# Optimization experiments

Hardware: AMD Instinct MI355X
Metric: run time of the kernel (lower is better)

Reference implementation:

```python
import jax, jax.numpy as jnp
import numpy as np

B, N = 32, 1024
NUM = B * N
DIMS = [(1, 128, 8), (128, 128, 8), (128, 64, 16), (64, 64, 16), (64, 32, 1)]  # (cin, cout, heads)

def _edges():
    # bidirectional chain per batch element, offset by N per graph (as in torch forward)
    a = np.arange(N - 1)
    offs = (np.arange(B) * N)[:, None]
    src = np.concatenate([(a[None] + offs).ravel(), (a[None] + 1 + offs).ravel()])
    dst = np.concatenate([(a[None] + 1 + offs).ravel(), (a[None] + offs).ravel()])
    return jnp.asarray(src, jnp.int32), jnp.asarray(dst, jnp.int32)

def _conv(x, src, dst, Wm, bm, Ws, bs, att):
    # PyG GeneralConv: directed msg, additive attention, aggr='add', head-mean, + lin_self
    h, cout = att.shape
    m = (x @ Wm + bm)[src].reshape(-1, h, cout)          # [E, H, C] edge messages
    m = jnp.where(m > 0, m, 0.01 * m)                    # F.leaky_relu default slope 0.01
    alpha = jnp.einsum('ehc,hc->eh', m, att)             # [E, H] attention logits
    amax = jax.ops.segment_max(alpha, dst, num_segments=NUM)
    ex = jnp.exp(alpha - amax[dst])
    den = jax.ops.segment_sum(ex, dst, num_segments=NUM)
    w = ex / (den[dst] + 1e-16)                          # segment softmax over incoming edges
    agg = jax.ops.segment_sum(m * w[:, :, None], dst, num_segments=NUM)  # [NUM, H, C]
    return agg.mean(axis=1) + x @ Ws + bs                # head mean + self loop linear

def _forward(nodes, params, Wc, bc):
    src, dst = _edges()
    x = nodes.reshape(NUM, 1)
    for i, p in enumerate(params):
        x = _conv(x, src, dst, *p)
        if i < 4:
            x = jax.nn.elu(x)                            # Dropout(0.4) identity at eval
    out = x.reshape(B, N, -1)[:, -1, :]                  # last node per graph -> [B, 32]
    return out @ Wc + bc, out

def setup_inputs():
    key = jax.random.key(0)
    ks = jax.random.split(key, 20)
    inp = {"nodes": jax.random.normal(ks[0], (B, N), dtype=jnp.float32)}
    i = 1
    for l, (cin, cout, h) in enumerate(DIMS, 1):
        s = float(1.0 / np.sqrt(cin))
        inp["Wm%d" % l] = jax.random.uniform(ks[i], (cin, h * cout), jnp.float32, -s, s); i += 1
        inp["bm%d" % l] = jnp.zeros((h * cout,), jnp.float32)
        inp["Ws%d" % l] = jax.random.uniform(ks[i], (cin, cout), jnp.float32, -s, s); i += 1
        inp["bs%d" % l] = jnp.zeros((cout,), jnp.float32)
        inp["att%d" % l] = jax.random.normal(ks[i], (h, cout), jnp.float32) * 0.1; i += 1
    inp["Wc"] = jax.random.normal(ks[i], (32, 1), jnp.float32) * 0.1
    inp["bc"] = jnp.zeros((1,), jnp.float32)
    return inp

def reference(nodes, Wm1, bm1, Ws1, bs1, att1, Wm2, bm2, Ws2, bs2, att2, Wm3, bm3, Ws3, bs3, att3, Wm4, bm4, Ws4, bs4, att4, Wm5, bm5, Ws5, bs5, att5, Wc, bc):
    params = [(Wm1, bm1, Ws1, bs1, att1), (Wm2, bm2, Ws2, bs2, att2), (Wm3, bm3, Ws3, bs3, att3), (Wm4, bm4, Ws4, bs4, att4), (Wm5, bm5, Ws5, bs5, att5)]
    return _forward(nodes, params, Wc, bc)
```

## Files before the change

### kernel.cpp

```cpp
#include <hip/hip_runtime.h>

#define BATCH 32
#define NLEN  1024
#define NUMV  (BATCH * NLEN)

typedef __attribute__((ext_vector_type(8))) short short8;
typedef __attribute__((ext_vector_type(4))) float f32x4;

__device__ inline unsigned short rne_bf16(float x) {
    union { float f; unsigned u; } a; a.f = x;
    return (unsigned short)((a.u + 0x7FFFu + ((a.u >> 16) & 1u)) >> 16);
}
__device__ inline void bsplit(float x, unsigned short& h, unsigned short& l) {
    union { float f; unsigned u; } a; a.f = x;
    unsigned hb = (a.u + 0x7FFFu + ((a.u >> 16) & 1u)) & 0xFFFF0000u;
    h = (unsigned short)(hb >> 16);
    union { unsigned u; float f; } hf; hf.u = hb;
    l = rne_bf16(x - hf.f);
}
__device__ inline float bf16_to_f(unsigned short v) {
    union { unsigned u; float f; } a; a.u = ((unsigned)v) << 16; return a.f;
}

template<int N> __device__ __forceinline__ void wait_vmcnt() {
    if constexpr (N == 0)      asm volatile("s_waitcnt vmcnt(0)" ::: "memory");
    else if constexpr (N == 1) asm volatile("s_waitcnt vmcnt(1)" ::: "memory");
    else if constexpr (N == 2) asm volatile("s_waitcnt vmcnt(2)" ::: "memory");
    else if constexpr (N == 4) asm volatile("s_waitcnt vmcnt(4)" ::: "memory");
    else static_assert(N == 0 || N == 1 || N == 2 || N == 4, "");
}

template<int CIN, int COUT, int H>
__device__ void pack_layer(const float* __restrict__ Wm, const float* __restrict__ Ws,
                           unsigned short* __restrict__ out, int t0, int nthr)
{
    constexpr int HC = H * COUT;
    constexpr int KC = ((CIN + 31) & ~31) / 32;
    constexpr int NT = (HC + COUT) / 16;
    const int total = NT * KC * 1024;
    for (int f = t0; f < total; f += nthr) {
        int j  = f & 7;
        int c  = (f >> 3) & 15;
        int g  = (f >> 7) & 3;
        int hl = (f >> 9) & 1;
        int r2 = f >> 10;
        int kc = r2 % KC, nt = r2 / KC;
        int k = kc * 32 + g * 8 + j, col = nt * 16 + c;
        float v = 0.f;
        if (k < CIN) v = (col < HC) ? Wm[k * HC + col] : Ws[k * COUT + (col - HC)];
        unsigned short h, l; bsplit(v, h, l);
        out[f] = hl ? l : h;
    }
}

__global__ void pack_all(const float* Wm1, const float* Ws1, const float* Wm2, const float* Ws2,
                         const float* Wm3, const float* Ws3, const float* Wm4, const float* Ws4,
                         unsigned short* p1, unsigned short* p2, unsigned short* p3, unsigned short* p4)
{
    int t = blockIdx.x * 256 + threadIdx.x;
    int n = gridDim.x * 256;
    pack_layer<1, 128, 8>(Wm1, Ws1, p1, t, n);
    pack_layer<128, 128, 8>(Wm2, Ws2, p2, t, n);
    pack_layer<128, 64, 16>(Wm3, Ws3, p3, t, n);
    pack_layer<64, 64, 16>(Wm4, Ws4, p4, t, n);
}

template<int CIN, int COUT, int H, bool MPACK>
__global__ __launch_bounds__(256, 3)
void conv_reg(const float* __restrict__ x, const unsigned short* __restrict__ pw,
              const float* __restrict__ bm, const float* __restrict__ bs,
              const float* __restrict__ att, float* __restrict__ y)
{
    constexpr int HC = H * COUT;
    static_assert(HC == 1024, "");
    constexpr int KC   = ((CIN + 31) & ~31) / 32;
    constexpr int HT   = COUT / 16;
    constexpr int MT   = HC / 16;
    constexpr int CPH  = 2 * KC * 128;
    constexpr int ROWSB = 56;
    constexpr int TPG  = (NLEN + ROWSB - 1) / ROWSB;
    constexpr int PL   = HC + COUT;
    constexpr float invH = 1.0f / H;

    const int tid  = threadIdx.x;
    const int lane = tid & 63;
    const int w    = tid >> 6;
    const int r    = lane & 15;
    const int gg   = lane >> 4;
    const int g    = blockIdx.x / TPG;
    const int n0   = (blockIdx.x % TPG) * ROWSB;
    const size_t gstart = (size_t)g * NLEN;

    __shared__ alignas(16) unsigned short bufs[2][2 * KC * 1024];
    __shared__ alignas(8) float pl[PL * 2];

    for (int i = tid; i < PL; i += 256) {
        float a, b;
        if (i < HC) { a = bm[i]; b = att[i]; }
        else        { a = bs[i - HC]; b = 0.f; }
        pl[2 * i] = a; pl[2 * i + 1] = b;
    }

    short8 a_hi[KC], a_lo[KC];
    {
        const int na = n0 - 1 + w * 14 + r;
        const bool av = (na >= 0) && (na < NLEN);
        const float* xrow = x + (gstart + (size_t)(av ? na : 0)) * CIN;
        #pragma unroll
        for (int kc = 0; kc < KC; kc++) {
            float vals[8];
            if constexpr (CIN % 32 == 0) {
                if (av) {
                    f32x4 v0 = *(const f32x4*)(xrow + kc * 32 + gg * 8);
                    f32x4 v1 = *(const f32x4*)(xrow + kc * 32 + gg * 8 + 4);
                    vals[0]=v0[0]; vals[1]=v0[1]; vals[2]=v0[2]; vals[3]=v0[3];
                    vals[4]=v1[0]; vals[5]=v1[1]; vals[6]=v1[2]; vals[7]=v1[3];
                } else {
                    #pragma unroll
                    for (int jj = 0; jj < 8; jj++) vals[jj] = 0.f;
                }
            } else {
                #pragma unroll
                for (int jj = 0; jj < 8; jj++) {
                    int k = kc * 32 + gg * 8 + jj;
                    vals[jj] = (av && k < CIN) ? xrow[k] : 0.f;
                }
            }
            union { short8 v; unsigned short u[8]; } hu, lu;
            #pragma unroll
            for (int jj = 0; jj < 8; jj++) bsplit(vals[jj], hu.u[jj], lu.u[jj]);
            a_hi[kc] = hu.v; a_lo[kc] = lu.v;
        }
    }

    auto issue_half = [&](int hh, int par) {
        const size_t cbase = (size_t)hh * CPH;
        #pragma unroll
        for (int i = 0; i < KC; i++) {
            const int chunk0 = (w * KC + i) * 64;
            const unsigned short* gsrc = pw + (cbase + chunk0 + lane) * 8;
            unsigned short* ldst = &bufs[par][chunk0 * 8];
            __builtin_amdgcn_global_load_lds(
                (const __attribute__((address_space(1))) void*)gsrc,
                (__attribute__((address_space(3))) void*)ldst,
                16, 0, 0);
        }
    };

    float out[HT][4];
    #pragma unroll
    for (int q = 0; q < HT; q++)
        #pragma unroll
        for (int e = 0; e < 4; e++) out[q][e] = 0.f;

    float    mf[MPACK ? 1 : HT][4];
    unsigned mpk[MPACK ? HT : 1][2];

    issue_half(0, 0);
    issue_half(1, 1);
    asm volatile("s_waitcnt lgkmcnt(0)" ::: "memory");

    const int boff = gg * 128 + r * 8;

    for (int h = 0; h < H; h++) {
        float p[4] = {0.f, 0.f, 0.f, 0.f};
        #pragma unroll
        for (int hq = 0; hq < HT / 2; hq++) {
            const int par = hq & 1;
            const int hh  = h * (HT / 2) + hq;
            wait_vmcnt<KC>();
            __builtin_amdgcn_s_barrier();
            __builtin_amdgcn_sched_barrier(0);
            #pragma unroll
            for (int t2 = 0; t2 < 2; t2++) {
                const int q   = hq * 2 + t2;
                const int nt  = h * HT + q;
                const int col = nt * 16 + r;
                const float2 pv = *(const float2*)&pl[col * 2];
                short8 bh[KC], bl[KC];
                #pragma unroll
                for (int kc = 0; kc < KC; kc++) {
                    bh[kc] = *(const short8*)&bufs[par][t2 * KC * 1024 + (kc * 2 + 0) * 512 + boff];
                    bl[kc] = *(const short8*)&bufs[par][t2 * KC * 1024 + (kc * 2 + 1) * 512 + boff];
                }
                f32x4 acc0 = {pv.x, pv.x, pv.x, pv.x};
                f32x4 acc1 = {0.f, 0.f, 0.f, 0.f};
                f32x4 acc2 = {0.f, 0.f, 0.f, 0.f};
                #pragma unroll
                for (int kc = 0; kc < KC; kc++) {
                    acc0 = __builtin_amdgcn_mfma_f32_16x16x32_bf16(a_hi[kc], bh[kc], acc0, 0, 0, 0);
                    acc1 = __builtin_amdgcn_mfma_f32_16x16x32_bf16(a_hi[kc], bl[kc], acc1, 0, 0, 0);
                    acc2 = __builtin_amdgcn_mfma_f32_16x16x32_bf16(a_lo[kc], bh[kc], acc2, 0, 0, 0);
                }
                float vv[4];
                #pragma unroll
                for (int e = 0; e < 4; e++) {
                    float v = acc0[e] + acc1[e] + acc2[e];
                    v = v > 0.f ? v : 0.01f * v;
                    vv[e] = v;
                    p[e] += v * pv.y;
                }
                if constexpr (MPACK) {
                    mpk[q][0] = ((unsigned)rne_bf16(vv[1]) << 16) | rne_bf16(vv[0]);
                    mpk[q][1] = ((unsigned)rne_bf16(vv[3]) << 16) | rne_bf16(vv[2]);
                } else {
                    #pragma unroll
                    for (int e = 0; e < 4; e++) mf[q][e] = vv[e];
                }
            }
            __builtin_amdgcn_sched_barrier(0);
            __builtin_amdgcn_s_barrier();
            __builtin_amdgcn_sched_barrier(0);
            issue_half(hh + 2, par);
        }
        #pragma unroll
        for (int e = 0; e < 4; e++) {
            float v = p[e];
            v += __shfl_xor(v, 1, 64);
            v += __shfl_xor(v, 2, 64);
            v += __shfl_xor(v, 4, 64);
            v += __shfl_xor(v, 8, 64);
            p[e] = v;
        }
        {
            const int jbase = w * 14;
            float a3u = __shfl_up(p[3], 16, 64);
            float a0d = __shfl_down(p[0], 16, 64);
            float wpv[4], wnv[4];
            #pragma unroll
            for (int e = 0; e < 4; e++) {
                const int jr = gg * 4 + e;
                const int nl = n0 - 1 + jbase + jr;
                const bool hp = nl >= 1;
                const bool hn = nl < NLEN - 1;
                float ap = (e > 0) ? p[e - 1] : a3u;
                float an = (e < 3) ? p[e + 1] : a0d;
                float apx = hp ? ap : -1e30f;
                float anx = hn ? an : -1e30f;
                float mx = fmaxf(apx, anx);
                float ep = hp ? __expf(ap - mx) : 0.f;
                float en = hn ? __expf(an - mx) : 0.f;
                float inv = 1.f / (ep + en + 1e-16f);
                wpv[e] = ep * inv; wnv[e] = en * inv;
            }
            #pragma unroll
            for (int q = 0; q < HT; q++) {
                float v0, v1, v2, v3;
                if constexpr (MPACK) {
                    v0 = bf16_to_f((unsigned short)(mpk[q][0] & 0xffff));
                    v1 = bf16_to_f((unsigned short)(mpk[q][0] >> 16));
                    v2 = bf16_to_f((unsigned short)(mpk[q][1] & 0xffff));
                    v3 = bf16_to_f((unsigned short)(mpk[q][1] >> 16));
                } else {
                    v0 = mf[q][0]; v1 = mf[q][1]; v2 = mf[q][2]; v3 = mf[q][3];
                }
                float m3u = __shfl_up(v3, 16, 64);
                float m0d = __shfl_down(v0, 16, 64);
                float mvals[4] = {v0, v1, v2, v3};
                #pragma unroll
                for (int e = 0; e < 4; e++) {
                    float mprev = (e > 0) ? mvals[e - 1] : m3u;
                    float mnext = (e < 3) ? mvals[e + 1] : m0d;
                    out[q][e] += wpv[e] * mprev + wnv[e] * mnext;
                }
            }
        }
    }

    #pragma unroll
    for (int q2h = 0; q2h < HT / 2; q2h++) {
        const int hh  = MT / 2 + q2h;
        const int par = q2h & 1;
        if (q2h < HT / 2 - 1) wait_vmcnt<KC>(); else wait_vmcnt<0>();
        __builtin_amdgcn_s_barrier();
        __builtin_amdgcn_sched_barrier(0);
        #pragma unroll
        for (int t2 = 0; t2 < 2; t2++) {
            const int q2 = q2h * 2 + t2;
            const int c2 = q2 * 16 + r;
            const float bsv = pl[(HC + c2) * 2];
            short8 bh[KC], bl[KC];
            #pragma unroll
            for (int kc = 0; kc < KC; kc++) {
                bh[kc] = *(const short8*)&bufs[par][t2 * KC * 1024 + (kc * 2 + 0) * 512 + boff];
                bl[kc] = *(const short8*)&bufs[par][t2 * KC * 1024 + (kc * 2 + 1) * 512 + boff];
            }
            f32x4 acc0 = {bsv, bsv, bsv, bsv};
            f32x4 acc1 = {0.f, 0.f, 0.f, 0.f};
            f32x4 acc2 = {0.f, 0.f, 0.f, 0.f};
            #pragma unroll
            for (int kc = 0; kc < KC; kc++) {
                acc0 = __builtin_amdgcn_mfma_f32_16x16x32_bf16(a_hi[kc], bh[kc], acc0, 0, 0, 0);
                acc1 = __builtin_amdgcn_mfma_f32_16x16x32_bf16(a_hi[kc], bl[kc], acc1, 0, 0, 0);
                acc2 = __builtin_amdgcn_mfma_f32_16x16x32_bf16(a_lo[kc], bh[kc], acc2, 0, 0, 0);
            }
            const int jbase = w * 14;
            #pragma unroll
            for (int e = 0; e < 4; e++) {
                const int jr = gg * 4 + e;
                const int nl = n0 - 1 + jbase + jr;
                float v = out[q2][e] * invH + (acc0[e] + acc1[e] + acc2[e]);
                v = v > 0.f ? v : __expf(v) - 1.f;
                if (jr >= 1 && jr <= 14 && nl < NLEN)
                    y[(gstart + nl) * COUT + c2] = v;
            }
        }
        __builtin_amdgcn_sched_barrier(0);
        __builtin_amdgcn_s_barrier();
        __builtin_amdgcn_sched_barrier(0);
        if (q2h + 2 < HT / 2) issue_half(hh + 2, par);
    }
}

__global__ void final_head(const float* __restrict__ x4,
                           const float* __restrict__ Wm,
                           const float* __restrict__ bm,
                           const float* __restrict__ Ws,
                           const float* __restrict__ bs,
                           const float* __restrict__ Wc,
                           const float* __restrict__ bc,
                           float* __restrict__ out)
{
    int g = blockIdx.x;
    int c = threadIdx.x;
    const float* xu = &x4[((long)g * NLEN + NLEN - 2) * 64];
    const float* xv = xu + 64;
    float o = 0.f;
    if (c < 32) {
        float m = bm[c];
        float s = bs[c];
        for (int k = 0; k < 64; k++) {
            m = fmaf(xu[k], Wm[k * 32 + c], m);
            s = fmaf(xv[k], Ws[k * 32 + c], s);
        }
        m = m > 0.f ? m : 0.01f * m;
        o = m + s;
        out[32 + g * 32 + c] = o;
    }
    float tsum = (c < 32) ? o * Wc[c] : 0.f;
    #pragma unroll
    for (int sft = 16; sft > 0; sft >>= 1)
        tsum += __shfl_xor(tsum, sft, 64);
    if (c == 0) out[g] = tsum + bc[0];
}

extern "C" void kernel_launch(void* const* d_in, const int* in_sizes, int n_in,
                              void* d_out, int out_size, void* d_ws, size_t ws_size,
                              hipStream_t stream)
{
    const float* nodes = (const float*)d_in[0];
    auto L = [&](int l, int k) { return (const float*)d_in[1 + (l - 1) * 5 + k]; };

    float* xb0 = (float*)d_ws;
    float* xb1 = xb0 + (size_t)NUMV * 128;
    unsigned short* p1 = (unsigned short*)(xb1 + (size_t)NUMV * 128);
    unsigned short* p2 = p1 + 72 * 1024;
    unsigned short* p3 = p2 + 72 * 4096;
    unsigned short* p4 = p3 + 68 * 4096;

    pack_all<<<dim3(512), dim3(256), 0, stream>>>(
        L(1,0), L(1,2), L(2,0), L(2,2), L(3,0), L(3,2), L(4,0), L(4,2), p1, p2, p3, p4);

    constexpr int TPG = (NLEN + 55) / 56;
    dim3 grid(BATCH * TPG);
    dim3 blk(256);

    conv_reg<1,   128, 8,  false><<<grid, blk, 0, stream>>>(nodes, p1, L(1,1), L(1,3), L(1,4), xb0);
    conv_reg<128, 128, 8,  true ><<<grid, blk, 0, stream>>>(xb0,   p2, L(2,1), L(2,3), L(2,4), xb1);
    conv_reg<128, 64,  16, false><<<grid, blk, 0, stream>>>(xb1,   p3, L(3,1), L(3,3), L(3,4), xb0);
    conv_reg<64,  64,  16, false><<<grid, blk, 0, stream>>>(xb0,   p4, L(4,1), L(4,3), L(4,4), xb1);

    final_head<<<dim3(BATCH), dim3(64), 0, stream>>>(
        xb1, L(5,0), L(5,1), L(5,2), L(5,3),
        (const float*)d_in[26], (const float*)d_in[27], (float*)d_out);
}
```

Baseline: 389.1 us.

## Load packed weight tiles directly into registers instead of LDS staging

Removes the LDS double buffer filled by global_load_lds, together with its block-wide barriers and vmcnt waits. Each wave now loads B fragments for each weight tile straight from global memory into registers, prefetching one tile ahead in a two-register-buffer ping-pong. This drops the LDS traffic and the synchronisation between waves. In exchange, every wave issues its own global reads of the same weights, which may rely on L1/L2 hits, and register pressure goes up under the launch bound.

Measured after the change: 397.6 us. 1.02x slower.

```diff
diff --git a/kernel.cpp b/kernel.cpp
--- a/kernel.cpp
+++ b/kernel.cpp
@@ -20,14 +20,6 @@
 }
 __device__ inline float bf16_to_f(unsigned short v) {
     union { unsigned u; float f; } a; a.u = ((unsigned)v) << 16; return a.f;
-}
-
-template<int N> __device__ __forceinline__ void wait_vmcnt() {
-    if constexpr (N == 0)      asm volatile("s_waitcnt vmcnt(0)" ::: "memory");
-    else if constexpr (N == 1) asm volatile("s_waitcnt vmcnt(1)" ::: "memory");
-    else if constexpr (N == 2) asm volatile("s_waitcnt vmcnt(2)" ::: "memory");
-    else if constexpr (N == 4) asm volatile("s_waitcnt vmcnt(4)" ::: "memory");
-    else static_assert(N == 0 || N == 1 || N == 2 || N == 4, "");
 }
 
 template<int CIN, int COUT, int H>
@@ -76,7 +68,7 @@
     constexpr int KC   = ((CIN + 31) & ~31) / 32;
     constexpr int HT   = COUT / 16;
     constexpr int MT   = HC / 16;
-    constexpr int CPH  = 2 * KC * 128;
+    constexpr int NTOT = MT + HT;
     constexpr int ROWSB = 56;
     constexpr int TPG  = (NLEN + ROWSB - 1) / ROWSB;
     constexpr int PL   = HC + COUT;
@@ -91,7 +83,6 @@
     const int n0   = (blockIdx.x % TPG) * ROWSB;
     const size_t gstart = (size_t)g * NLEN;
 
-    __shared__ alignas(16) unsigned short bufs[2][2 * KC * 1024];
     __shared__ alignas(8) float pl[PL * 2];
 
     for (int i = tid; i < PL; i += 256) {
@@ -133,20 +124,6 @@
         }
     }
 
-    auto issue_half = [&](int hh, int par) {
-        const size_t cbase = (size_t)hh * CPH;
-        #pragma unroll
-        for (int i = 0; i < KC; i++) {
-            const int chunk0 = (w * KC + i) * 64;
-            const unsigned short* gsrc = pw + (cbase + chunk0 + lane) * 8;
-            unsigned short* ldst = &bufs[par][chunk0 * 8];
-            __builtin_amdgcn_global_load_lds(
-                (const __attribute__((address_space(1))) void*)gsrc,
-                (__attribute__((address_space(3))) void*)ldst,
-                16, 0, 0);
-        }
-    };
-
     float out[HT][4];
     #pragma unroll
     for (int q = 0; q < HT; q++)
@@ -156,62 +133,65 @@
     float    mf[MPACK ? 1 : HT][4];
     unsigned mpk[MPACK ? HT : 1][2];
 
-    issue_half(0, 0);
-    issue_half(1, 1);
-    asm volatile("s_waitcnt lgkmcnt(0)" ::: "memory");
+    __syncthreads();
 
     const int boff = gg * 128 + r * 8;
+
+    short8 b0h[KC], b0l[KC], b1h[KC], b1l[KC];
+
+    auto loadB = [&](short8 (&dh)[KC], short8 (&dl)[KC], int nt) {
+        const unsigned short* tb = pw + (size_t)nt * (KC * 1024);
+        #pragma unroll
+        for (int kc = 0; kc < KC; kc++) {
+            dh[kc] = *(const short8*)&tb[(kc * 2 + 0) * 512 + boff];
+            dl[kc] = *(const short8*)&tb[(kc * 2 + 1) * 512 + boff];
+        }
+    };
+    auto mfma3 = [&](short8 (&bh)[KC], short8 (&bl)[KC], float seed) -> f32x4 {
+        f32x4 acc0 = {seed, seed, seed, seed};
+        f32x4 acc1 = {0.f, 0.f, 0.f, 0.f};
+        f32x4 acc2 = {0.f, 0.f, 0.f, 0.f};
+        #pragma unroll
+        for (int kc = 0; kc < KC; kc++) {
+            acc0 = __builtin_amdgcn_mfma_f32_16x16x32_bf16(a_hi[kc], bh[kc], acc0, 0, 0, 0);
+            acc1 = __builtin_amdgcn_mfma_f32_16x16x32_bf16(a_hi[kc], bl[kc], acc1, 0, 0, 0);
+            acc2 = __builtin_amdgcn_mfma_f32_16x16x32_bf16(a_lo[kc], bh[kc], acc2, 0, 0, 0);
+        }
+        return acc0 + acc1 + acc2;
+    };
+    auto msgTile = [&](short8 (&bh)[KC], short8 (&bl)[KC], int nt, float (&p)[4]) -> f32x4 {
+        const float2 pv = *(const float2*)&pl[(nt * 16 + r) * 2];
+        f32x4 vv = mfma3(bh, bl, pv.x);
+        #pragma unroll
+        for (int e = 0; e < 4; e++) {
+            float v = vv[e];
+            v = v > 0.f ? v : 0.01f * v;
+            vv[e] = v;
+            p[e] += v * pv.y;
+        }
+        return vv;
+    };
+    auto storeM = [&](int q, f32x4 vv) {
+        if constexpr (MPACK) {
+            mpk[q][0] = ((unsigned)rne_bf16(vv[1]) << 16) | rne_bf16(vv[0]);
+            mpk[q][1] = ((unsigned)rne_bf16(vv[3]) << 16) | rne_bf16(vv[2]);
+        } else {
+            #pragma unroll
+            for (int e = 0; e < 4; e++) mf[q][e] = vv[e];
+        }
+    };
+
+    loadB(b0h, b0l, 0);
 
     for (int h = 0; h < H; h++) {
         float p[4] = {0.f, 0.f, 0.f, 0.f};
         #pragma unroll
-        for (int hq = 0; hq < HT / 2; hq++) {
-            const int par = hq & 1;
-            const int hh  = h * (HT / 2) + hq;
-            wait_vmcnt<KC>();
-            __builtin_amdgcn_s_barrier();
-            __builtin_amdgcn_sched_barrier(0);
-            #pragma unroll
-            for (int t2 = 0; t2 < 2; t2++) {
-                const int q   = hq * 2 + t2;
-                const int nt  = h * HT + q;
-                const int col = nt * 16 + r;
-                const float2 pv = *(const float2*)&pl[col * 2];
-                short8 bh[KC], bl[KC];
-                #pragma unroll
-                for (int kc = 0; kc < KC; kc++) {
-                    bh[kc] = *(const short8*)&bufs[par][t2 * KC * 1024 + (kc * 2 + 0) * 512 + boff];
-                    bl[kc] = *(const short8*)&bufs[par][t2 * KC * 1024 + (kc * 2 + 1) * 512 + boff];
-                }
-                f32x4 acc0 = {pv.x, pv.x, pv.x, pv.x};
-                f32x4 acc1 = {0.f, 0.f, 0.f, 0.f};
-                f32x4 acc2 = {0.f, 0.f, 0.f, 0.f};
-                #pragma unroll
-                for (int kc = 0; kc < KC; kc++) {
-                    acc0 = __builtin_amdgcn_mfma_f32_16x16x32_bf16(a_hi[kc], bh[kc], acc0, 0, 0, 0);
-                    acc1 = __builtin_amdgcn_mfma_f32_16x16x32_bf16(a_hi[kc], bl[kc], acc1, 0, 0, 0);
-                    acc2 = __builtin_amdgcn_mfma_f32_16x16x32_bf16(a_lo[kc], bh[kc], acc2, 0, 0, 0);
-                }
-                float vv[4];
-                #pragma unroll
-                for (int e = 0; e < 4; e++) {
-                    float v = acc0[e] + acc1[e] + acc2[e];
-                    v = v > 0.f ? v : 0.01f * v;
-                    vv[e] = v;
-                    p[e] += v * pv.y;
-                }
-                if constexpr (MPACK) {
-                    mpk[q][0] = ((unsigned)rne_bf16(vv[1]) << 16) | rne_bf16(vv[0]);
-                    mpk[q][1] = ((unsigned)rne_bf16(vv[3]) << 16) | rne_bf16(vv[2]);
-                } else {
-                    #pragma unroll
-                    for (int e = 0; e < 4; e++) mf[q][e] = vv[e];
-                }
-            }
-            __builtin_amdgcn_sched_barrier(0);
-            __builtin_amdgcn_s_barrier();
-            __builtin_amdgcn_sched_barrier(0);
-            issue_half(hh + 2, par);
+        for (int qq = 0; qq < HT; qq += 2) {
+            const int nt0 = h * HT + qq;
+            loadB(b1h, b1l, nt0 + 1);
+            storeM(qq, msgTile(b0h, b0l, nt0, p));
+            if (nt0 + 2 < NTOT) loadB(b0h, b0l, nt0 + 2);
+            storeM(qq + 1, msgTile(b1h, b1l, nt0 + 1, p));
         }
         #pragma unroll
         for (int e = 0; e < 4; e++) {
@@ -267,48 +247,28 @@
         }
     }
 
+    auto selfTile = [&](short8 (&bh)[KC], short8 (&bl)[KC], int q2) {
+        const int c2 = q2 * 16 + r;
+        const float bsv = pl[(HC + c2) * 2];
+        f32x4 acc = mfma3(bh, bl, bsv);
+        const int jbase = w * 14;
+        #pragma unroll
+        for (int e = 0; e < 4; e++) {
+            const int jr = gg * 4 + e;
+            const int nl = n0 - 1 + jbase + jr;
+            float v = out[q2][e] * invH + acc[e];
+            v = v > 0.f ? v : __expf(v) - 1.f;
+            if (jr >= 1 && jr <= 14 && nl < NLEN)
+                y[(gstart + nl) * COUT + c2] = v;
+        }
+    };
     #pragma unroll
-    for (int q2h = 0; q2h < HT / 2; q2h++) {
-        const int hh  = MT / 2 + q2h;
-        const int par = q2h & 1;
-        if (q2h < HT / 2 - 1) wait_vmcnt<KC>(); else wait_vmcnt<0>();
-        __builtin_amdgcn_s_barrier();
-        __builtin_amdgcn_sched_barrier(0);
-        #pragma unroll
-        for (int t2 = 0; t2 < 2; t2++) {
-            const int q2 = q2h * 2 + t2;
-            const int c2 = q2 * 16 + r;
-            const float bsv = pl[(HC + c2) * 2];
-            short8 bh[KC], bl[KC];
-            #pragma unroll
-            for (int kc = 0; kc < KC; kc++) {
-                bh[kc] = *(const short8*)&bufs[par][t2 * KC * 1024 + (kc * 2 + 0) * 512 + boff];
-                bl[kc] = *(const short8*)&bufs[par][t2 * KC * 1024 + (kc * 2 + 1) * 512 + boff];
-            }
-            f32x4 acc0 = {bsv, bsv, bsv, bsv};
-            f32x4 acc1 = {0.f, 0.f, 0.f, 0.f};
-            f32x4 acc2 = {0.f, 0.f, 0.f, 0.f};
-            #pragma unroll
-            for (int kc = 0; kc < KC; kc++) {
-                acc0 = __builtin_amdgcn_mfma_f32_16x16x32_bf16(a_hi[kc], bh[kc], acc0, 0, 0, 0);
-                acc1 = __builtin_amdgcn_mfma_f32_16x16x32_bf16(a_hi[kc], bl[kc], acc1, 0, 0, 0);
-                acc2 = __builtin_amdgcn_mfma_f32_16x16x32_bf16(a_lo[kc], bh[kc], acc2, 0, 0, 0);
-            }
-            const int jbase = w * 14;
-            #pragma unroll
-            for (int e = 0; e < 4; e++) {
-                const int jr = gg * 4 + e;
-                const int nl = n0 - 1 + jbase + jr;
-                float v = out[q2][e] * invH + (acc0[e] + acc1[e] + acc2[e]);
-                v = v > 0.f ? v : __expf(v) - 1.f;
-                if (jr >= 1 && jr <= 14 && nl < NLEN)
-                    y[(gstart + nl) * COUT + c2] = v;
-            }
-        }
-        __builtin_amdgcn_sched_barrier(0);
-        __builtin_amdgcn_s_barrier();
-        __builtin_amdgcn_sched_barrier(0);
-        if (q2h + 2 < HT / 2) issue_half(hh + 2, par);
+    for (int q2 = 0; q2 < HT; q2 += 2) {
+        const int nt0 = MT + q2;
+        loadB(b1h, b1l, nt0 + 1);
+        selfTile(b0h, b0l, q2);
+        if (nt0 + 2 < NTOT) loadB(b0h, b0l, nt0 + 2);
+        selfTile(b1h, b1l, q2 + 1);
     }
 }
 
```
